# Optimization experiments

Measured on AMD Instinct MI355X. Metric: run time of the kernel, lower is better.

Reference implementation:

```python
import math
import jax
import jax.numpy as jnp
import numpy as np

N_NODE = 50000
N_EDGE = 1_600_000
D_IN = 128
D_K = 32
N_HEADS = 8


def setup_inputs() -> dict:
    key = jax.random.key(0)
    k_h, k_e, k_q, k_k, k_v = jax.random.split(key, 5)
    h = jax.random.normal(k_h, (N_NODE, D_IN), dtype=jnp.float32)
    edge_idx = jax.random.randint(k_e, (2, N_EDGE), 0, N_NODE, dtype=jnp.int64)
    scale = 1.0 / math.sqrt(D_IN)
    WQ = jax.random.normal(k_q, (N_HEADS, D_IN, D_K), dtype=jnp.float32) * scale
    WK = jax.random.normal(k_k, (N_HEADS, D_IN, D_K), dtype=jnp.float32) * scale
    WV = jax.random.normal(k_v, (N_HEADS, D_IN, D_K), dtype=jnp.float32) * scale
    return {"h": h, "edge_idx": edge_idx, "WQ": WQ, "WK": WK, "WV": WV}


def reference(h, edge_idx, WQ, WK, WV):
    n_node = h.shape[0]
    d_k = WK.shape[-1]
    # Per-head projections: [H, N, d]
    Q = jnp.einsum('nd,hdk->hnk', h, WQ)
    K = jnp.einsum('nd,hdk->hnk', h, WK)
    V = jnp.einsum('nd,hdv->hnv', h, WV)
    row = edge_idx[0]  # destination (softmax normalized per row, dim=1)
    col = edge_idx[1]  # source
    # Edge logits: e[h, e] = <Q[h, row[e]], K[h, col[e]]> / sqrt(d_k)
    e = jnp.einsum('hek,hek->he', Q[:, row, :], K[:, col, :]) / jnp.sqrt(
        jnp.asarray(d_k, dtype=h.dtype))
    eT = e.T  # [E, H]
    # Sparse (segment) softmax over outgoing edges of each row node.
    m = jax.ops.segment_max(eT, row, num_segments=n_node)  # [N, H]
    m = jnp.where(jnp.isfinite(m), m, jnp.zeros_like(m))   # guard empty rows
    ex = jnp.exp(eT - m[row])                               # [E, H]
    denom = jax.ops.segment_sum(ex, row, num_segments=n_node)  # [N, H]
    att = ex / denom[row]                                   # [E, H]
    # Sparse mm: out[i] = sum_{edges (i,j)} att * V[j]
    msgs = att[:, :, None] * jnp.transpose(V, (1, 0, 2))[col]  # [E, H, d_v]
    out = jax.ops.segment_sum(msgs, row, num_segments=n_node)  # [N, H, d_v]
    # aggregate == 'concat' -> head-major concat along feature dim
    return out.reshape(n_node, -1)
```

## Files before the change

kernel.cpp:

```cpp
#include <hip/hip_runtime.h>
#include <hip/hip_bf16.h>
#include <cstdint>

#define D_IN 128
#define DK 32
#define NH 8
#define HD 256
#define KVW 512

typedef __attribute__((ext_vector_type(8))) short short8;
typedef __attribute__((ext_vector_type(4))) float f32x4;

__device__ inline float bf2f(unsigned short u) {
  union { unsigned int i; float f; } c;
  c.i = ((unsigned int)u) << 16;
  return c.f;
}
__device__ inline float u2f(unsigned int u) {
  union { unsigned int i; float f; } c; c.i = u; return c.f;
}
__device__ inline short f2bf(float f) {
  union { float f; unsigned int i; } c; c.f = f;
  unsigned int u = c.i;
  u = u + 0x7FFFu + ((u >> 16) & 1u);
  return (short)(u >> 16);
}

__global__ __launch_bounds__(256) void prep_w_kernel(
    const float* __restrict__ WQ, const float* __restrict__ WK,
    const float* __restrict__ WV, short8* __restrict__ Bbuf) {
  int ct = blockIdx.x;
  int t = threadIdx.x;
  int kt = t >> 6, L = t & 63;
  int col = ct * 16 + (L & 15);
  int type = col >> 8;
  const float* W = (type == 0) ? WQ : (type == 1) ? WK : WV;
  int head = (col & 255) >> 5;
  int kk = col & 31;
  int k0 = kt * 32 + ((L >> 4) << 3);
  short8 o;
  #pragma unroll
  for (int r = 0; r < 8; r++)
    o[r] = f2bf(W[head * (D_IN * DK) + (k0 + r) * DK + kk]);
  Bbuf[(size_t)(ct * 4 + kt) * 64 + L] = o;
}

__global__ __launch_bounds__(256) void gemm_qkv_kernel(
    const float* __restrict__ h, const short8* __restrict__ Bbuf,
    __hip_bfloat16* __restrict__ Q, __hip_bfloat16* __restrict__ KV,
    int nt_total) {
  __shared__ float hs[16][132];
  __shared__ short lds[16][768];
  int nt = blockIdx.x;
  int t = threadIdx.x;
  {
    const float4* h4 = (const float4*)(h + (size_t)nt * 16 * 128);
    float4 v0 = h4[t * 2], v1 = h4[t * 2 + 1];
    int node = t >> 4, dim = (t & 15) * 8;
    hs[node][dim + 0] = v0.x; hs[node][dim + 1] = v0.y;
    hs[node][dim + 2] = v0.z; hs[node][dim + 3] = v0.w;
    hs[node][dim + 4] = v1.x; hs[node][dim + 5] = v1.y;
    hs[node][dim + 6] = v1.z; hs[node][dim + 7] = v1.w;
  }
  __syncthreads();
  int w = t >> 6;
  int L = t & 63;
  int arow = L & 15, k0base = ((L >> 4) << 3);
  short8 afrag[4];
  #pragma unroll
  for (int kt = 0; kt < 4; kt++) {
    #pragma unroll
    for (int r = 0; r < 8; r++)
      afrag[kt][r] = f2bf(hs[arow][kt * 32 + k0base + r]);
  }
  f32x4 acc[12];
  #pragma unroll
  for (int c = 0; c < 12; c++) acc[c] = (f32x4){0.f, 0.f, 0.f, 0.f};
  #pragma unroll
  for (int kt = 0; kt < 4; kt++) {
    #pragma unroll
    for (int c = 0; c < 12; c++) {
      short8 b = Bbuf[(size_t)((w * 12 + c) * 4 + kt) * 64 + L];
      acc[c] = __builtin_amdgcn_mfma_f32_16x16x32_bf16(afrag[kt], b, acc[c], 0, 0, 0);
    }
  }
  int row0 = (L >> 4) << 2;
  int col0 = w * 192 + (L & 15);
  #pragma unroll
  for (int c = 0; c < 12; c++) {
    #pragma unroll
    for (int r = 0; r < 4; r++)
      lds[row0 + r][col0 + c * 16] = f2bf(acc[c][r]);
  }
  __syncthreads();
  #pragma unroll
  for (int j = 0; j < 2; j++) {
    int u = t + j * 256;
    int row = u >> 5, uc = u & 31;
    float4 vdat = *(const float4*)&lds[row][uc * 8];
    *(float4*)(Q + (size_t)(nt * 16 + row) * HD + uc * 8) = vdat;
  }
  #pragma unroll
  for (int j = 0; j < 4; j++) {
    int u = t + j * 256;
    int row = u >> 6, uc = u & 63;
    float4 vdat = *(const float4*)&lds[row][256 + uc * 8];
    *(float4*)(KV + (size_t)(nt * 16 + row) * KVW + uc * 8) = vdat;
  }
}

__global__ void rank_kernel(const int* __restrict__ row, int n_edge,
                            int* __restrict__ cnt, int* __restrict__ rank) {
  int i = blockIdx.x * blockDim.x + threadIdx.x;
  if (i < n_edge) rank[i] = atomicAdd(&cnt[row[i]], 1);
}

__global__ __launch_bounds__(256) void scan1_kernel(
    const int* __restrict__ cnt, int n, int* __restrict__ exc,
    int* __restrict__ bsum) {
  __shared__ int s[256];
  int gid = blockIdx.x * 256 + threadIdx.x;
  int v = (gid < n) ? cnt[gid] : 0;
  s[threadIdx.x] = v;
  __syncthreads();
  #pragma unroll
  for (int off = 1; off < 256; off <<= 1) {
    int t = (threadIdx.x >= off) ? s[threadIdx.x - off] : 0;
    __syncthreads();
    s[threadIdx.x] += t;
    __syncthreads();
  }
  if (gid < n) exc[gid] = s[threadIdx.x] - v;
  if (threadIdx.x == 255) bsum[blockIdx.x] = s[255];
}

__global__ __launch_bounds__(256) void scan2_kernel(int* __restrict__ bsum,
                                                    int nb) {
  __shared__ int s[256];
  int v = (threadIdx.x < nb) ? bsum[threadIdx.x] : 0;
  s[threadIdx.x] = v;
  __syncthreads();
  #pragma unroll
  for (int off = 1; off < 256; off <<= 1) {
    int t = (threadIdx.x >= off) ? s[threadIdx.x - off] : 0;
    __syncthreads();
    s[threadIdx.x] += t;
    __syncthreads();
  }
  if (threadIdx.x < nb) bsum[threadIdx.x] = s[threadIdx.x] - v;
}

__global__ __launch_bounds__(256) void scan3_kernel(
    int* __restrict__ exc, const int* __restrict__ bsum, int n, int n_edge) {
  int gid = blockIdx.x * 256 + threadIdx.x;
  if (gid < n) exc[gid] = exc[gid] + bsum[blockIdx.x];
  if (gid == 0) exc[n] = n_edge;
}

__global__ void scatter_kernel(const int* __restrict__ row,
                               const int* __restrict__ col,
                               const int* __restrict__ rank, int n_edge,
                               const int* __restrict__ offsets,
                               int* __restrict__ col_sorted) {
  int i = blockIdx.x * blockDim.x + threadIdx.x;
  if (i < n_edge) col_sorted[offsets[row[i]] + rank[i]] = col[i];
}

#define AT_PROCESS(r)                                                        \
  {                                                                          \
    float x0 = u2f(r.x << 16), x1 = u2f(r.x & 0xFFFF0000u);                  \
    float x2 = u2f(r.y << 16), x3 = u2f(r.y & 0xFFFF0000u);                  \
    float x4 = u2f(r.z << 16), x5 = u2f(r.z & 0xFFFF0000u);                  \
    float x6 = u2f(r.w << 16), x7 = u2f(r.w & 0xFFFF0000u);                  \
    float d = x0 * qf0;                                                      \
    d = fmaf(x1, qf1, d); d = fmaf(x2, qf2, d); d = fmaf(x3, qf3, d);        \
    d = fmaf(x4, qf4, d); d = fmaf(x5, qf5, d); d = fmaf(x6, qf6, d);        \
    d = fmaf(x7, qf7, d);                                                    \
    d += __shfl_xor(d, 1);                                                   \
    d += __shfl_xor(d, 2);                                                   \
    float lg = __shfl(d, sub);                                               \
    if (__any(lg - m > 8.0f)) {                                              \
      float nm = fmaxf(m, lg);                                               \
      float sc = __expf(m - nm);                                             \
      denom *= sc;                                                           \
      a0 *= sc; a1 *= sc; a2 *= sc; a3 *= sc;                                \
      a4 *= sc; a5 *= sc; a6 *= sc; a7 *= sc;                                \
      m = nm;                                                                \
    }                                                                        \
    float p = __expf(lg - m);                                                \
    denom += p;                                                              \
    a0 = fmaf(p, x0, a0); a1 = fmaf(p, x1, a1);                              \
    a2 = fmaf(p, x2, a2); a3 = fmaf(p, x3, a3);                              \
    a4 = fmaf(p, x4, a4); a5 = fmaf(p, x5, a5);                              \
    a6 = fmaf(p, x6, a6); a7 = fmaf(p, x7, a7);                              \
  }

__global__ __launch_bounds__(256) void attn_kernel(
    const __hip_bfloat16* __restrict__ Q, const __hip_bfloat16* __restrict__ KV,
    const int* __restrict__ offsets, const int* __restrict__ col_sorted,
    float* __restrict__ out, int n_node) {
  int wave = threadIdx.x >> 6;
  int lane = threadIdx.x & 63;
  int sub = lane & 31;
  int node = blockIdx.x * 4 + wave;
  if (node >= n_node) return;
  int start = offsets[node], end = offsets[node + 1];

  const float QS = 0.17677669529663687f;
  float qf0, qf1, qf2, qf3, qf4, qf5, qf6, qf7;
  {
    uint4 qr = *(const uint4*)(Q + (size_t)node * HD + sub * 8);
    qf0 = u2f(qr.x << 16) * QS; qf1 = u2f(qr.x & 0xFFFF0000u) * QS;
    qf2 = u2f(qr.y << 16) * QS; qf3 = u2f(qr.y & 0xFFFF0000u) * QS;
    qf4 = u2f(qr.z << 16) * QS; qf5 = u2f(qr.z & 0xFFFF0000u) * QS;
    qf6 = u2f(qr.w << 16) * QS; qf7 = u2f(qr.w & 0xFFFF0000u) * QS;
  }
  float m = -INFINITY, denom = 0.f;
  float a0 = 0.f, a1 = 0.f, a2 = 0.f, a3 = 0.f;
  float a4 = 0.f, a5 = 0.f, a6 = 0.f, a7 = 0.f;

  const char* kvbase = (const char*)KV + lane * 16;
  int e = start;
  for (; e + 4 <= end; e += 4) {
    int c0 = col_sorted[e], c1 = col_sorted[e + 1];
    int c2 = col_sorted[e + 2], c3 = col_sorted[e + 3];
    uint4 r0 = *(const uint4*)(kvbase + (size_t)c0 * 1024);
    uint4 r1 = *(const uint4*)(kvbase + (size_t)c1 * 1024);
    uint4 r2 = *(const uint4*)(kvbase + (size_t)c2 * 1024);
    uint4 r3 = *(const uint4*)(kvbase + (size_t)c3 * 1024);
    AT_PROCESS(r0);
    AT_PROCESS(r1);
    AT_PROCESS(r2);
    AT_PROCESS(r3);
  }
  for (; e < end; e++) {
    int c = col_sorted[e];
    uint4 r = *(const uint4*)(kvbase + (size_t)c * 1024);
    AT_PROCESS(r);
  }

  float inv = (end > start) ? 1.f / denom : 0.f;
  if (lane >= 32) {
    float* op = out + (size_t)node * HD + sub * 8;
    float4 o0 = make_float4(a0 * inv, a1 * inv, a2 * inv, a3 * inv);
    float4 o1 = make_float4(a4 * inv, a5 * inv, a6 * inv, a7 * inv);
    *(float4*)op = o0;
    *(float4*)(op + 4) = o1;
  }
}

extern "C" void kernel_launch(void* const* d_in, const int* in_sizes, int n_in,
                              void* d_out, int out_size, void* d_ws,
                              size_t ws_size, hipStream_t stream) {
  const float* h = (const float*)d_in[0];
  const int* edge = (const int*)d_in[1];
  const float* WQ = (const float*)d_in[2];
  const float* WK = (const float*)d_in[3];
  const float* WV = (const float*)d_in[4];
  float* out = (float*)d_out;

  int n_node = in_sizes[0] / D_IN;
  int n_edge = in_sizes[1] / 2;
  const int* row = edge;
  const int* col = edge + n_edge;

  char* ws = (char*)d_ws;
  size_t off = 0;
  auto alloc = [&](size_t bytes) {
    void* p = ws + off;
    off += (bytes + 255) & ~(size_t)255;
    return p;
  };
  int nt_total = (n_node + 15) / 16;
  __hip_bfloat16* Q = (__hip_bfloat16*)alloc((size_t)nt_total * 16 * HD * 2);
  __hip_bfloat16* KV = (__hip_bfloat16*)alloc((size_t)nt_total * 16 * KVW * 2);
  short8* Bbuf = (short8*)alloc((size_t)48 * 4 * 64 * 16);
  int* col_sorted = (int*)alloc((size_t)n_edge * 4);
  int* rank = (int*)alloc((size_t)n_edge * 4);
  int* cnt = (int*)alloc((size_t)n_node * 4);
  int* offsets = (int*)alloc((size_t)(n_node + 1) * 4);
  int* bsum = (int*)alloc(256 * 4);

  hipMemsetAsync(cnt, 0, (size_t)n_node * 4, stream);

  prep_w_kernel<<<48, 256, 0, stream>>>(WQ, WK, WV, Bbuf);
  gemm_qkv_kernel<<<nt_total, 256, 0, stream>>>(h, Bbuf, Q, KV, nt_total);

  int nb_e = (n_edge + 255) / 256;
  rank_kernel<<<nb_e, 256, 0, stream>>>(row, n_edge, cnt, rank);

  int nb = (n_node + 255) / 256;
  scan1_kernel<<<nb, 256, 0, stream>>>(cnt, n_node, offsets, bsum);
  scan2_kernel<<<1, 256, 0, stream>>>(bsum, nb);
  scan3_kernel<<<nb, 256, 0, stream>>>(offsets, bsum, n_node, n_edge);

  scatter_kernel<<<nb_e, 256, 0, stream>>>(row, col, rank, n_edge, offsets,
                                           col_sorted);

  attn_kernel<<<(n_node + 3) / 4, 256, 0, stream>>>(Q, KV, offsets, col_sorted,
                                                    out, n_node);
}
```

Before: 376.9 us.

## Merge weight prep with count zeroing, fuse GEMM with edge ranking, unroll attention by 8

Result: slower. 388.2 us (+3.0%).

```diff
diff --git a/kernel.cpp b/kernel.cpp
--- a/kernel.cpp
+++ b/kernel.cpp
@@ -26,29 +26,41 @@
   return (short)(u >> 16);
 }
 
-__global__ __launch_bounds__(256) void prep_w_kernel(
+__global__ __launch_bounds__(256) void prep_w_zero_kernel(
     const float* __restrict__ WQ, const float* __restrict__ WK,
-    const float* __restrict__ WV, short8* __restrict__ Bbuf) {
-  int ct = blockIdx.x;
-  int t = threadIdx.x;
-  int kt = t >> 6, L = t & 63;
-  int col = ct * 16 + (L & 15);
-  int type = col >> 8;
-  const float* W = (type == 0) ? WQ : (type == 1) ? WK : WV;
-  int head = (col & 255) >> 5;
-  int kk = col & 31;
-  int k0 = kt * 32 + ((L >> 4) << 3);
-  short8 o;
-  #pragma unroll
-  for (int r = 0; r < 8; r++)
-    o[r] = f2bf(W[head * (D_IN * DK) + (k0 + r) * DK + kk]);
-  Bbuf[(size_t)(ct * 4 + kt) * 64 + L] = o;
-}
-
-__global__ __launch_bounds__(256) void gemm_qkv_kernel(
+    const float* __restrict__ WV, short8* __restrict__ Bbuf,
+    int* __restrict__ cnt, int n_node) {
+  if (blockIdx.x < 48) {
+    int ct = blockIdx.x;
+    int t = threadIdx.x;
+    int kt = t >> 6, L = t & 63;
+    int col = ct * 16 + (L & 15);
+    int type = col >> 8;
+    const float* W = (type == 0) ? WQ : (type == 1) ? WK : WV;
+    int head = (col & 255) >> 5;
+    int kk = col & 31;
+    int k0 = kt * 32 + ((L >> 4) << 3);
+    short8 o;
+    #pragma unroll
+    for (int r = 0; r < 8; r++)
+      o[r] = f2bf(W[head * (D_IN * DK) + (k0 + r) * DK + kk]);
+    Bbuf[(size_t)(ct * 4 + kt) * 64 + L] = o;
+  } else {
+    int i = (blockIdx.x - 48) * 256 + threadIdx.x;
+    if (i < n_node) cnt[i] = 0;
+  }
+}
+
+__global__ __launch_bounds__(256) void gemm_rank_kernel(
     const float* __restrict__ h, const short8* __restrict__ Bbuf,
     __hip_bfloat16* __restrict__ Q, __hip_bfloat16* __restrict__ KV,
-    int nt_total) {
+    int nt_total, const int* __restrict__ row, int n_edge,
+    int* __restrict__ cnt, int* __restrict__ rank) {
+  if (blockIdx.x >= (unsigned)nt_total) {
+    int i = (blockIdx.x - nt_total) * 256 + threadIdx.x;
+    if (i < n_edge) rank[i] = atomicAdd(&cnt[row[i]], 1);
+    return;
+  }
   __shared__ float hs[16][132];
   __shared__ short lds[16][768];
   int nt = blockIdx.x;
@@ -96,23 +108,17 @@
   #pragma unroll
   for (int j = 0; j < 2; j++) {
     int u = t + j * 256;
-    int row = u >> 5, uc = u & 31;
-    float4 vdat = *(const float4*)&lds[row][uc * 8];
-    *(float4*)(Q + (size_t)(nt * 16 + row) * HD + uc * 8) = vdat;
+    int r2 = u >> 5, uc = u & 31;
+    float4 vdat = *(const float4*)&lds[r2][uc * 8];
+    *(float4*)(Q + (size_t)(nt * 16 + r2) * HD + uc * 8) = vdat;
   }
   #pragma unroll
   for (int j = 0; j < 4; j++) {
     int u = t + j * 256;
-    int row = u >> 6, uc = u & 63;
-    float4 vdat = *(const float4*)&lds[row][256 + uc * 8];
-    *(float4*)(KV + (size_t)(nt * 16 + row) * KVW + uc * 8) = vdat;
-  }
-}
-
-__global__ void rank_kernel(const int* __restrict__ row, int n_edge,
-                            int* __restrict__ cnt, int* __restrict__ rank) {
-  int i = blockIdx.x * blockDim.x + threadIdx.x;
-  if (i < n_edge) rank[i] = atomicAdd(&cnt[row[i]], 1);
+    int r2 = u >> 6, uc = u & 63;
+    float4 vdat = *(const float4*)&lds[r2][256 + uc * 8];
+    *(float4*)(KV + (size_t)(nt * 16 + r2) * KVW + uc * 8) = vdat;
+  }
 }
 
 __global__ __launch_bounds__(256) void scan1_kernel(
@@ -221,17 +227,30 @@
 
   const char* kvbase = (const char*)KV + lane * 16;
   int e = start;
+  for (; e + 8 <= end; e += 8) {
+    int c0 = col_sorted[e],     c1 = col_sorted[e + 1];
+    int c2 = col_sorted[e + 2], c3 = col_sorted[e + 3];
+    int c4 = col_sorted[e + 4], c5 = col_sorted[e + 5];
+    int c6 = col_sorted[e + 6], c7 = col_sorted[e + 7];
+    uint4 r0 = *(const uint4*)(kvbase + (size_t)c0 * 1024);
+    uint4 r1 = *(const uint4*)(kvbase + (size_t)c1 * 1024);
+    uint4 r2 = *(const uint4*)(kvbase + (size_t)c2 * 1024);
+    uint4 r3 = *(const uint4*)(kvbase + (size_t)c3 * 1024);
+    uint4 r4 = *(const uint4*)(kvbase + (size_t)c4 * 1024);
+    uint4 r5 = *(const uint4*)(kvbase + (size_t)c5 * 1024);
+    uint4 r6 = *(const uint4*)(kvbase + (size_t)c6 * 1024);
+    uint4 r7 = *(const uint4*)(kvbase + (size_t)c7 * 1024);
+    AT_PROCESS(r0); AT_PROCESS(r1); AT_PROCESS(r2); AT_PROCESS(r3);
+    AT_PROCESS(r4); AT_PROCESS(r5); AT_PROCESS(r6); AT_PROCESS(r7);
+  }
   for (; e + 4 <= end; e += 4) {
-    int c0 = col_sorted[e], c1 = col_sorted[e + 1];
+    int c0 = col_sorted[e],     c1 = col_sorted[e + 1];
     int c2 = col_sorted[e + 2], c3 = col_sorted[e + 3];
     uint4 r0 = *(const uint4*)(kvbase + (size_t)c0 * 1024);
     uint4 r1 = *(const uint4*)(kvbase + (size_t)c1 * 1024);
     uint4 r2 = *(const uint4*)(kvbase + (size_t)c2 * 1024);
     uint4 r3 = *(const uint4*)(kvbase + (size_t)c3 * 1024);
-    AT_PROCESS(r0);
-    AT_PROCESS(r1);
-    AT_PROCESS(r2);
-    AT_PROCESS(r3);
+    AT_PROCESS(r0); AT_PROCESS(r1); AT_PROCESS(r2); AT_PROCESS(r3);
   }
   for (; e < end; e++) {
     int c = col_sorted[e];
@@ -281,15 +300,14 @@
   int* offsets = (int*)alloc((size_t)(n_node + 1) * 4);
   int* bsum = (int*)alloc(256 * 4);
 
-  hipMemsetAsync(cnt, 0, (size_t)n_node * 4, stream);
-
-  prep_w_kernel<<<48, 256, 0, stream>>>(WQ, WK, WV, Bbuf);
-  gemm_qkv_kernel<<<nt_total, 256, 0, stream>>>(h, Bbuf, Q, KV, nt_total);
-
+  int nb = (n_node + 255) / 256;
   int nb_e = (n_edge + 255) / 256;
-  rank_kernel<<<nb_e, 256, 0, stream>>>(row, n_edge, cnt, rank);
-
-  int nb = (n_node + 255) / 256;
+
+  prep_w_zero_kernel<<<48 + nb, 256, 0, stream>>>(WQ, WK, WV, Bbuf, cnt,
+                                                  n_node);
+  gemm_rank_kernel<<<nt_total + nb_e, 256, 0, stream>>>(
+      h, Bbuf, Q, KV, nt_total, row, n_edge, cnt, rank);
+
   scan1_kernel<<<nb, 256, 0, stream>>>(cnt, n_node, offsets, bsum);
   scan2_kernel<<<1, 256, 0, stream>>>(bsum, nb);
   scan3_kernel<<<nb, 256, 0, stream>>>(offsets, bsum, n_node, n_edge);
```

## Double-buffer KV row gathers into LDS via async global_load_lds in attention

Applied to the files above, without the earlier changes.

After: 378.9 us. About the same (+0.5%).

```diff
diff --git a/kernel.cpp b/kernel.cpp
--- a/kernel.cpp
+++ b/kernel.cpp
@@ -11,11 +11,6 @@
 typedef __attribute__((ext_vector_type(8))) short short8;
 typedef __attribute__((ext_vector_type(4))) float f32x4;
 
-__device__ inline float bf2f(unsigned short u) {
-  union { unsigned int i; float f; } c;
-  c.i = ((unsigned int)u) << 16;
-  return c.f;
-}
 __device__ inline float u2f(unsigned int u) {
   union { unsigned int i; float f; } c; c.i = u; return c.f;
 }
@@ -24,6 +19,11 @@
   unsigned int u = c.i;
   u = u + 0x7FFFu + ((u >> 16) & 1u);
   return (short)(u >> 16);
+}
+__device__ inline void gll16(const void* gsrc, void* ldst) {
+  __builtin_amdgcn_global_load_lds(
+      (const __attribute__((address_space(1))) unsigned int*)gsrc,
+      (__attribute__((address_space(3))) unsigned int*)ldst, 16, 0, 0);
 }
 
 __global__ __launch_bounds__(256) void prep_w_kernel(
@@ -96,16 +96,16 @@
   #pragma unroll
   for (int j = 0; j < 2; j++) {
     int u = t + j * 256;
-    int row = u >> 5, uc = u & 31;
-    float4 vdat = *(const float4*)&lds[row][uc * 8];
-    *(float4*)(Q + (size_t)(nt * 16 + row) * HD + uc * 8) = vdat;
+    int r2 = u >> 5, uc = u & 31;
+    float4 vdat = *(const float4*)&lds[r2][uc * 8];
+    *(float4*)(Q + (size_t)(nt * 16 + r2) * HD + uc * 8) = vdat;
   }
   #pragma unroll
   for (int j = 0; j < 4; j++) {
     int u = t + j * 256;
-    int row = u >> 6, uc = u & 63;
-    float4 vdat = *(const float4*)&lds[row][256 + uc * 8];
-    *(float4*)(KV + (size_t)(nt * 16 + row) * KVW + uc * 8) = vdat;
+    int r2 = u >> 6, uc = u & 63;
+    float4 vdat = *(const float4*)&lds[r2][256 + uc * 8];
+    *(float4*)(KV + (size_t)(nt * 16 + r2) * KVW + uc * 8) = vdat;
   }
 }
 
@@ -166,7 +166,7 @@
   if (i < n_edge) col_sorted[offsets[row[i]] + rank[i]] = col[i];
 }
 
-#define AT_PROCESS(r)                                                        \
+#define AT_PROCESS(r, valid)                                                 \
   {                                                                          \
     float x0 = u2f(r.x << 16), x1 = u2f(r.x & 0xFFFF0000u);                  \
     float x2 = u2f(r.y << 16), x3 = u2f(r.y & 0xFFFF0000u);                  \
@@ -179,6 +179,7 @@
     d += __shfl_xor(d, 1);                                                   \
     d += __shfl_xor(d, 2);                                                   \
     float lg = __shfl(d, sub);                                               \
+    lg = (valid) ? lg : -INFINITY;                                           \
     if (__any(lg - m > 8.0f)) {                                              \
       float nm = fmaxf(m, lg);                                               \
       float sc = __expf(m - nm);                                             \
@@ -199,6 +200,7 @@
     const __hip_bfloat16* __restrict__ Q, const __hip_bfloat16* __restrict__ KV,
     const int* __restrict__ offsets, const int* __restrict__ col_sorted,
     float* __restrict__ out, int n_node) {
+  __shared__ char kvbuf[4][2][4][1024];
   int wave = threadIdx.x >> 6;
   int lane = threadIdx.x & 63;
   int sub = lane & 31;
@@ -219,24 +221,44 @@
   float a0 = 0.f, a1 = 0.f, a2 = 0.f, a3 = 0.f;
   float a4 = 0.f, a5 = 0.f, a6 = 0.f, a7 = 0.f;
 
-  const char* kvbase = (const char*)KV + lane * 16;
-  int e = start;
-  for (; e + 4 <= end; e += 4) {
-    int c0 = col_sorted[e], c1 = col_sorted[e + 1];
-    int c2 = col_sorted[e + 2], c3 = col_sorted[e + 3];
-    uint4 r0 = *(const uint4*)(kvbase + (size_t)c0 * 1024);
-    uint4 r1 = *(const uint4*)(kvbase + (size_t)c1 * 1024);
-    uint4 r2 = *(const uint4*)(kvbase + (size_t)c2 * 1024);
-    uint4 r3 = *(const uint4*)(kvbase + (size_t)c3 * 1024);
-    AT_PROCESS(r0);
-    AT_PROCESS(r1);
-    AT_PROCESS(r2);
-    AT_PROCESS(r3);
-  }
-  for (; e < end; e++) {
-    int c = col_sorted[e];
-    uint4 r = *(const uint4*)(kvbase + (size_t)c * 1024);
-    AT_PROCESS(r);
+  char* myb = &kvbuf[wave][0][0][0];
+
+  for (int base = start; base < end; base += 64) {
+    int nn = min(64, end - base);
+    int myc = col_sorted[base + (lane < nn ? lane : 0)];
+    int ng = (nn + 3) >> 2;
+
+    auto issue = [&](int g) {
+      char* slotb = myb + (g & 1) * 4096;
+      #pragma unroll
+      for (int j = 0; j < 4; j++) {
+        int idx = g * 4 + j;
+        int c = __shfl(myc, idx < nn ? idx : 0, 64);
+        const char* src = (const char*)KV + (size_t)c * 1024 + lane * 16;
+        gll16(src, slotb + j * 1024);
+      }
+    };
+
+    issue(0);
+    if (ng > 1) issue(1);
+
+    for (int g = 0; g < ng; ++g) {
+      if (g + 1 < ng) {
+        asm volatile("s_waitcnt vmcnt(4)" ::: "memory");
+      } else {
+        asm volatile("s_waitcnt vmcnt(0)" ::: "memory");
+      }
+      __builtin_amdgcn_sched_barrier(0);
+      const char* slotb = myb + (g & 1) * 4096;
+      #pragma unroll
+      for (int j = 0; j < 4; j++) {
+        uint4 r = *(const uint4*)(slotb + j * 1024 + lane * 16);
+        bool valid = (g * 4 + j) < nn;
+        AT_PROCESS(r, valid);
+      }
+      __builtin_amdgcn_sched_barrier(0);
+      if (g + 2 < ng) issue(g + 2);
+    }
   }
 
   float inv = (end > start) ? 1.f / denom : 0.f;
```

## Split attention per head with head-major K/V layout and 4-edge-parallel waves

Applied to the files above, without the earlier changes.

Result: slower. 491.1 us (+30.3%).

```diff
diff --git a/kernel.cpp b/kernel.cpp
--- a/kernel.cpp
+++ b/kernel.cpp
@@ -6,18 +6,15 @@
 #define DK 32
 #define NH 8
 #define HD 256
-#define KVW 512
 
 typedef __attribute__((ext_vector_type(8))) short short8;
 typedef __attribute__((ext_vector_type(4))) float f32x4;
 
-__device__ inline float bf2f(unsigned short u) {
-  union { unsigned int i; float f; } c;
-  c.i = ((unsigned int)u) << 16;
-  return c.f;
-}
 __device__ inline float u2f(unsigned int u) {
   union { unsigned int i; float f; } c; c.i = u; return c.f;
+}
+__device__ inline float bfu(unsigned short u) {
+  union { unsigned int i; float f; } c; c.i = ((unsigned int)u) << 16; return c.f;
 }
 __device__ inline short f2bf(float f) {
   union { float f; unsigned int i; } c; c.f = f;
@@ -47,8 +44,8 @@
 
 __global__ __launch_bounds__(256) void gemm_qkv_kernel(
     const float* __restrict__ h, const short8* __restrict__ Bbuf,
-    __hip_bfloat16* __restrict__ Q, __hip_bfloat16* __restrict__ KV,
-    int nt_total) {
+    __hip_bfloat16* __restrict__ Qh, __hip_bfloat16* __restrict__ KVh,
+    int nt_total, int n_node) {
   __shared__ float hs[16][132];
   __shared__ short lds[16][768];
   int nt = blockIdx.x;
@@ -96,16 +93,19 @@
   #pragma unroll
   for (int j = 0; j < 2; j++) {
     int u = t + j * 256;
-    int row = u >> 5, uc = u & 31;
-    float4 vdat = *(const float4*)&lds[row][uc * 8];
-    *(float4*)(Q + (size_t)(nt * 16 + row) * HD + uc * 8) = vdat;
+    int hh = u >> 6, r2 = (u >> 2) & 15, part = u & 3;
+    float4 vdat = *(const float4*)&lds[r2][hh * 32 + part * 8];
+    *(float4*)(Qh + ((size_t)hh * n_node + nt * 16 + r2) * 32 + part * 8) = vdat;
   }
   #pragma unroll
   for (int j = 0; j < 4; j++) {
     int u = t + j * 256;
-    int row = u >> 6, uc = u & 63;
-    float4 vdat = *(const float4*)&lds[row][256 + uc * 8];
-    *(float4*)(KV + (size_t)(nt * 16 + row) * KVW + uc * 8) = vdat;
+    int hh = u >> 7, r2 = (u >> 3) & 15, part = u & 7;
+    int srccol = (part < 4) ? (256 + hh * 32 + part * 8)
+                            : (512 + hh * 32 + (part - 4) * 8);
+    float4 vdat = *(const float4*)&lds[r2][srccol];
+    *(float4*)(KVh + ((size_t)hh * n_node + nt * 16 + r2) * 64 +
+               ((part < 4) ? part * 8 : 32 + (part - 4) * 8)) = vdat;
   }
 }
 
@@ -166,86 +166,80 @@
   if (i < n_edge) col_sorted[offsets[row[i]] + rank[i]] = col[i];
 }
 
-#define AT_PROCESS(r)                                                        \
+__global__ __launch_bounds__(256) void attn_kernel(
+    const __hip_bfloat16* __restrict__ Qh, const __hip_bfloat16* __restrict__ KVh,
+    const int* __restrict__ offsets, const int* __restrict__ col_sorted,
+    float* __restrict__ out, int n_node) {
+  int head = blockIdx.x & 7;
+  int grp = blockIdx.x >> 3;
+  int wave = threadIdx.x >> 6;
+  int lane = threadIdx.x & 63;
+  int sub = lane & 15;
+  int eg = lane >> 4;
+  int node = grp * 4 + wave;
+  if (node >= n_node) return;
+  int start = offsets[node], end = offsets[node + 1];
+
+  const float QS = 0.17677669529663687f;
+  float qf0, qf1, qf2, qf3;
+  {
+    ushort4 qv = *(const ushort4*)(Qh + ((size_t)head * n_node + node) * 32 +
+                                   (sub & 7) * 4);
+    qf0 = bfu(qv.x) * QS; qf1 = bfu(qv.y) * QS;
+    qf2 = bfu(qv.z) * QS; qf3 = bfu(qv.w) * QS;
+  }
+  float m = -INFINITY, denom = 0.f;
+  float a0 = 0.f, a1 = 0.f, a2 = 0.f, a3 = 0.f;
+
+  const char* kvb = (const char*)KVh + (size_t)head * n_node * 128 + sub * 8;
+
+#define HP_EDGE(rr, vv)                                                      \
   {                                                                          \
-    float x0 = u2f(r.x << 16), x1 = u2f(r.x & 0xFFFF0000u);                  \
-    float x2 = u2f(r.y << 16), x3 = u2f(r.y & 0xFFFF0000u);                  \
-    float x4 = u2f(r.z << 16), x5 = u2f(r.z & 0xFFFF0000u);                  \
-    float x6 = u2f(r.w << 16), x7 = u2f(r.w & 0xFFFF0000u);                  \
+    float x0 = bfu(rr.x), x1 = bfu(rr.y), x2 = bfu(rr.z), x3 = bfu(rr.w);    \
     float d = x0 * qf0;                                                      \
     d = fmaf(x1, qf1, d); d = fmaf(x2, qf2, d); d = fmaf(x3, qf3, d);        \
-    d = fmaf(x4, qf4, d); d = fmaf(x5, qf5, d); d = fmaf(x6, qf6, d);        \
-    d = fmaf(x7, qf7, d);                                                    \
     d += __shfl_xor(d, 1);                                                   \
     d += __shfl_xor(d, 2);                                                   \
-    float lg = __shfl(d, sub);                                               \
-    if (__any(lg - m > 8.0f)) {                                              \
-      float nm = fmaxf(m, lg);                                               \
+    d += __shfl_xor(d, 4);                                                   \
+    float tt = __shfl_xor(d, 8);                                             \
+    float lg = (sub < 8) ? d : tt;                                           \
+    lg = (vv) ? lg : -INFINITY;                                              \
+    float cm = fmaxf(lg, __shfl_xor(lg, 16));                                \
+    cm = fmaxf(cm, __shfl_xor(cm, 32));                                      \
+    if (__any(cm - m > 8.0f)) {                                              \
+      float nm = fmaxf(m, cm);                                               \
       float sc = __expf(m - nm);                                             \
       denom *= sc;                                                           \
       a0 *= sc; a1 *= sc; a2 *= sc; a3 *= sc;                                \
-      a4 *= sc; a5 *= sc; a6 *= sc; a7 *= sc;                                \
       m = nm;                                                                \
     }                                                                        \
     float p = __expf(lg - m);                                                \
     denom += p;                                                              \
     a0 = fmaf(p, x0, a0); a1 = fmaf(p, x1, a1);                              \
     a2 = fmaf(p, x2, a2); a3 = fmaf(p, x3, a3);                              \
-    a4 = fmaf(p, x4, a4); a5 = fmaf(p, x5, a5);                              \
-    a6 = fmaf(p, x6, a6); a7 = fmaf(p, x7, a7);                              \
-  }
-
-__global__ __launch_bounds__(256) void attn_kernel(
-    const __hip_bfloat16* __restrict__ Q, const __hip_bfloat16* __restrict__ KV,
-    const int* __restrict__ offsets, const int* __restrict__ col_sorted,
-    float* __restrict__ out, int n_node) {
-  int wave = threadIdx.x >> 6;
-  int lane = threadIdx.x & 63;
-  int sub = lane & 31;
-  int node = blockIdx.x * 4 + wave;
-  if (node >= n_node) return;
-  int start = offsets[node], end = offsets[node + 1];
-
-  const float QS = 0.17677669529663687f;
-  float qf0, qf1, qf2, qf3, qf4, qf5, qf6, qf7;
-  {
-    uint4 qr = *(const uint4*)(Q + (size_t)node * HD + sub * 8);
-    qf0 = u2f(qr.x << 16) * QS; qf1 = u2f(qr.x & 0xFFFF0000u) * QS;
-    qf2 = u2f(qr.y << 16) * QS; qf3 = u2f(qr.y & 0xFFFF0000u) * QS;
-    qf4 = u2f(qr.z << 16) * QS; qf5 = u2f(qr.z & 0xFFFF0000u) * QS;
-    qf6 = u2f(qr.w << 16) * QS; qf7 = u2f(qr.w & 0xFFFF0000u) * QS;
-  }
-  float m = -INFINITY, denom = 0.f;
-  float a0 = 0.f, a1 = 0.f, a2 = 0.f, a3 = 0.f;
-  float a4 = 0.f, a5 = 0.f, a6 = 0.f, a7 = 0.f;
-
-  const char* kvbase = (const char*)KV + lane * 16;
-  int e = start;
-  for (; e + 4 <= end; e += 4) {
-    int c0 = col_sorted[e], c1 = col_sorted[e + 1];
-    int c2 = col_sorted[e + 2], c3 = col_sorted[e + 3];
-    uint4 r0 = *(const uint4*)(kvbase + (size_t)c0 * 1024);
-    uint4 r1 = *(const uint4*)(kvbase + (size_t)c1 * 1024);
-    uint4 r2 = *(const uint4*)(kvbase + (size_t)c2 * 1024);
-    uint4 r3 = *(const uint4*)(kvbase + (size_t)c3 * 1024);
-    AT_PROCESS(r0);
-    AT_PROCESS(r1);
-    AT_PROCESS(r2);
-    AT_PROCESS(r3);
-  }
-  for (; e < end; e++) {
-    int c = col_sorted[e];
-    uint4 r = *(const uint4*)(kvbase + (size_t)c * 1024);
-    AT_PROCESS(r);
-  }
+  }
+
+  for (int base = start; base < end; base += 8) {
+    int i0 = base + eg, i1 = base + 4 + eg;
+    bool v0 = i0 < end, v1 = i1 < end;
+    int c0 = col_sorted[v0 ? i0 : start];
+    int c1 = col_sorted[v1 ? i1 : start];
+    ushort4 r0 = *(const ushort4*)(kvb + (size_t)c0 * 128);
+    ushort4 r1 = *(const ushort4*)(kvb + (size_t)c1 * 128);
+    HP_EDGE(r0, v0);
+    HP_EDGE(r1, v1);
+  }
+
+  denom += __shfl_xor(denom, 16); denom += __shfl_xor(denom, 32);
+  a0 += __shfl_xor(a0, 16); a0 += __shfl_xor(a0, 32);
+  a1 += __shfl_xor(a1, 16); a1 += __shfl_xor(a1, 32);
+  a2 += __shfl_xor(a2, 16); a2 += __shfl_xor(a2, 32);
+  a3 += __shfl_xor(a3, 16); a3 += __shfl_xor(a3, 32);
 
   float inv = (end > start) ? 1.f / denom : 0.f;
-  if (lane >= 32) {
-    float* op = out + (size_t)node * HD + sub * 8;
-    float4 o0 = make_float4(a0 * inv, a1 * inv, a2 * inv, a3 * inv);
-    float4 o1 = make_float4(a4 * inv, a5 * inv, a6 * inv, a7 * inv);
-    *(float4*)op = o0;
-    *(float4*)(op + 4) = o1;
+  if (lane >= 8 && lane < 16) {
+    float4 o = make_float4(a0 * inv, a1 * inv, a2 * inv, a3 * inv);
+    *(float4*)(out + (size_t)node * HD + head * 32 + (sub - 8) * 4) = o;
   }
 }
 
@@ -272,8 +266,8 @@
     return p;
   };
   int nt_total = (n_node + 15) / 16;
-  __hip_bfloat16* Q = (__hip_bfloat16*)alloc((size_t)nt_total * 16 * HD * 2);
-  __hip_bfloat16* KV = (__hip_bfloat16*)alloc((size_t)nt_total * 16 * KVW * 2);
+  __hip_bfloat16* Qh = (__hip_bfloat16*)alloc((size_t)NH * n_node * 32 * 2);
+  __hip_bfloat16* KVh = (__hip_bfloat16*)alloc((size_t)NH * n_node * 64 * 2);
   short8* Bbuf = (short8*)alloc((size_t)48 * 4 * 64 * 16);
   int* col_sorted = (int*)alloc((size_t)n_edge * 4);
   int* rank = (int*)alloc((size_t)n_edge * 4);
@@ -284,7 +278,8 @@
   hipMemsetAsync(cnt, 0, (size_t)n_node * 4, stream);
 
   prep_w_kernel<<<48, 256, 0, stream>>>(WQ, WK, WV, Bbuf);
-  gemm_qkv_kernel<<<nt_total, 256, 0, stream>>>(h, Bbuf, Q, KV, nt_total);
+  gemm_qkv_kernel<<<nt_total, 256, 0, stream>>>(h, Bbuf, Qh, KVh, nt_total,
+                                                n_node);
 
   int nb_e = (n_edge + 255) / 256;
   rank_kernel<<<nb_e, 256, 0, stream>>>(row, n_edge, cnt, rank);
@@ -297,6 +292,6 @@
   scatter_kernel<<<nb_e, 256, 0, stream>>>(row, col, rank, n_edge, offsets,
                                            col_sorted);
 
-  attn_kernel<<<(n_node + 3) / 4, 256, 0, stream>>>(Q, KV, offsets, col_sorted,
-                                                    out, n_node);
-}
+  attn_kernel<<<((n_node + 3) / 4) * 8, 256, 0, stream>>>(
+      Qh, KVh, offsets, col_sorted, out, n_node);
+}
```
